# Kernel tuning notes

Hardware: AMD Instinct MI355X
Metric: run time of the kernel (lower is better)

Reference implementation:

```python
import jax, jax.numpy as jnp
import numpy as np

N = 4096
K = 3          # from loss_name 'LMNN-3'
MU = 0.5       # default mu in LMNN
NUM_CLASSES = 10


def setup_inputs() -> dict:
    key = jax.random.key(0)
    k1, k2 = jax.random.split(key)
    distances_sq = jax.random.uniform(k1, (N, N), dtype=jnp.float32)
    labels = jax.random.randint(k2, (N, 1), 0, NUM_CLASSES, dtype=jnp.int32)
    return {"distances_sq": distances_sq, "labels": labels}


def lmnn(D, labels, k=K, mu=MU):
    n = D.shape[0]
    same = (labels == labels.T).astype(D.dtype)              # [n,n] same-class indicator
    cross = same * (1.0 - jnp.eye(n, dtype=D.dtype))         # exclude self-pairs
    order = jnp.argsort(D, axis=-1)                          # ascending per row
    pull_mask = jnp.take_along_axis(cross, order, axis=-1)[:, : k + 1]   # [n,k+1]
    sortD = jnp.take_along_axis(D, order, axis=-1)[:, : k + 1]           # [n,k+1]
    pull_d = sortD * pull_mask                               # masked k+1 nearest distances
    pull = jnp.sum(pull_d)
    # push: sum_{i,m,j} relu((pull_d[i,m] - D[j,i] + 1) * pull_mask[i,m] * (1 - same[j,i]))
    # vectorized form of the original per-row Python loop; hinge is [n, k+1, n]
    hinge = jax.nn.relu(
        (pull_d[:, :, None] - D.T[:, None, :] + 1.0)
        * pull_mask[:, :, None]
        * (1.0 - same.T)[:, None, :]
    )
    push = jnp.sum(hinge)
    return (1.0 - mu) * pull + mu * push


def reference(distances_sq, labels):
    # grad_reverse is identity in the forward pass
    return lmnn(distances_sq, labels)
```

## Files before the change

kernel.cpp:

```cpp
#include <hip/hip_runtime.h>

#define N 4096
#define NCLS 10
#define RPB 4
#define NBLK (N / RPB)
#define CRG 16
#define CRC (NBLK / CRG)

__device__ __forceinline__ bool lessvi(float v1, int i1, float v2, int i2) {
    return (v1 < v2) || (v1 == v2 && i1 < i2);
}

__global__ __launch_bounds__(256, 4) void fused(const float* __restrict__ D,
                                                const int* __restrict__ labels,
                                                float* __restrict__ pdiff,
                                                float* __restrict__ pd_sum,
                                                float* __restrict__ a_cnt) {
    __shared__ float sv[RPB][16];
    __shared__ int   si[RPB][16];

    const int tid  = threadIdx.x;
    const int lane = tid & 63;
    const int wave = tid >> 6;
    const int r0   = blockIdx.x * RPB;

    int4 cl[4];
#pragma unroll
    for (int q = 0; q < 4; ++q) cl[q] = ((const int4*)labels)[tid + 256 * q];

    float4 diff[4] = {{0,0,0,0},{0,0,0,0},{0,0,0,0},{0,0,0,0}};

    const float4* rp = (const float4*)(D + (size_t)r0 * N);
    float4 vc[4], vn[4];
#pragma unroll
    for (int q = 0; q < 4; ++q) vc[q] = rp[tid + 256 * q];

#pragma unroll
    for (int r = 0; r < RPB; ++r) {
        if (r < RPB - 1) {
            const float4* np = rp + (size_t)(r + 1) * (N / 4);
#pragma unroll
            for (int q = 0; q < 4; ++q) vn[q] = np[tid + 256 * q];
        }
        const int row    = r0 + r;
        const int rowlab = labels[row];

        float tv[4] = {INFINITY, INFINITY, INFINITY, INFINITY};
        int   ti[4] = {0x7ffffff0, 0x7ffffff1, 0x7ffffff2, 0x7ffffff3};
#pragma unroll
        for (int q = 0; q < 4; ++q) {
            const float4 v = vc[q];
            diff[q].x += (cl[q].x != rowlab) ? v.x : 0.f;
            diff[q].y += (cl[q].y != rowlab) ? v.y : 0.f;
            diff[q].z += (cl[q].z != rowlab) ? v.z : 0.f;
            diff[q].w += (cl[q].w != rowlab) ? v.w : 0.f;

            const int c0 = 4 * tid + 1024 * q;
            const float vals[4] = {v.x, v.y, v.z, v.w};
#pragma unroll
            for (int e = 0; e < 4; ++e) {
                const float vv = vals[e];
                const int   ci = c0 + e;
                if (lessvi(vv, ci, tv[3], ti[3])) {
                    tv[3] = vv; ti[3] = ci;
#pragma unroll
                    for (int q2 = 3; q2 > 0; --q2) {
                        const bool sw = lessvi(tv[q2], ti[q2], tv[q2-1], ti[q2-1]);
                        const float av = tv[q2-1]; const int ai = ti[q2-1];
                        tv[q2-1] = sw ? tv[q2] : av;
                        ti[q2-1] = sw ? ti[q2] : ai;
                        tv[q2]   = sw ? av : tv[q2];
                        ti[q2]   = sw ? ai : ti[q2];
                    }
                }
            }
        }

#pragma unroll
        for (int off = 1; off < 64; off <<= 1) {
            float yv[4]; int yi[4];
#pragma unroll
            for (int k = 0; k < 4; ++k) {
                yv[k] = __shfl_xor(tv[k], off);
                yi[k] = __shfl_xor(ti[k], off);
            }
            float rv[4]; int ri[4];
#pragma unroll
            for (int k = 0; k < 4; ++k) {
                const bool tm = lessvi(tv[0], ti[0], yv[0], yi[0]);
                rv[k] = tm ? tv[0] : yv[0];
                ri[k] = tm ? ti[0] : yi[0];
#pragma unroll
                for (int q2 = 0; q2 < 3; ++q2) {
                    tv[q2] = tm ? tv[q2 + 1] : tv[q2];
                    ti[q2] = tm ? ti[q2 + 1] : ti[q2];
                    yv[q2] = tm ? yv[q2]     : yv[q2 + 1];
                    yi[q2] = tm ? yi[q2]     : yi[q2 + 1];
                }
            }
#pragma unroll
            for (int k = 0; k < 4; ++k) { tv[k] = rv[k]; ti[k] = ri[k]; }
        }

        if (lane == 0) {
#pragma unroll
            for (int k = 0; k < 4; ++k) {
                sv[r][wave * 4 + k] = tv[k];
                si[r][wave * 4 + k] = ti[k];
            }
        }

#pragma unroll
        for (int q = 0; q < 4; ++q) vc[q] = vn[q];
    }

    float4* op = (float4*)(pdiff + (size_t)blockIdx.x * N);
#pragma unroll
    for (int q = 0; q < 4; ++q) op[tid + 256 * q] = diff[q];

    __syncthreads();
    if (tid < RPB) {
        float bv[4] = {INFINITY, INFINITY, INFINITY, INFINITY};
        int   bi[4] = {0x7ffffff0, 0x7ffffff1, 0x7ffffff2, 0x7ffffff3};
#pragma unroll
        for (int k = 0; k < 16; ++k) {
            const float vv = sv[tid][k];
            const int   ci = si[tid][k];
            if (lessvi(vv, ci, bv[3], bi[3])) {
                bv[3] = vv; bi[3] = ci;
#pragma unroll
                for (int q2 = 3; q2 > 0; --q2) {
                    const bool sw = lessvi(bv[q2], bi[q2], bv[q2-1], bi[q2-1]);
                    const float av = bv[q2-1]; const int ai = bi[q2-1];
                    bv[q2-1] = sw ? bv[q2] : av;
                    bi[q2-1] = sw ? bi[q2] : ai;
                    bv[q2]   = sw ? av : bv[q2];
                    bi[q2]   = sw ? ai : bi[q2];
                }
            }
        }
        const int row = r0 + tid;
        const int li  = labels[row];
        float pd = 0.f, a = 0.f;
#pragma unroll
        for (int m = 0; m < 4; ++m) {
            const int j = bi[m];
            if (j != row && labels[j] == li) { pd += bv[m]; a += 1.f; }
        }
        pd_sum[row] = pd;
        a_cnt[row]  = a;
    }
}

__global__ __launch_bounds__(256) void col_reduce(const float* __restrict__ pdiff,
                                                  float* __restrict__ cdiff) {
    const int tile = blockIdx.x & 3;
    const int g    = blockIdx.x >> 2;
    const int col  = tile * 1024 + threadIdx.x * 4;
    float4 acc = {0.f, 0.f, 0.f, 0.f};
#pragma unroll 8
    for (int ch = 0; ch < CRC; ++ch) {
        const float4 v = *(const float4*)(pdiff + (size_t)(g * CRC + ch) * N + col);
        acc.x += v.x; acc.y += v.y; acc.z += v.z; acc.w += v.w;
    }
    *(float4*)(cdiff + (size_t)g * N + col) = acc;
}

__global__ __launch_bounds__(256) void finalize(const int* __restrict__ labels,
                                                const float* __restrict__ pd_sum,
                                                const float* __restrict__ a_cnt,
                                                const float* __restrict__ cdiff,
                                                float* __restrict__ out) {
    __shared__ int    cnt[NCLS];
    __shared__ double red[256];
    const int tid = threadIdx.x;

    if (tid < NCLS) cnt[tid] = 0;
    __syncthreads();
    for (int i = tid; i < N; i += 256) atomicAdd(&cnt[labels[i]], 1);
    __syncthreads();

    double acc = 0.0;
    for (int i = tid; i < N; i += 256) {
        const int li = labels[i];
        const double pd = (double)pd_sum[i];
        const double a  = (double)a_cnt[i];
        float csf = 0.f;
#pragma unroll
        for (int g = 0; g < CRG; ++g) csf += cdiff[(size_t)g * N + i];
        const double cs = (double)csf;
        const double cd = (double)(N - cnt[li]);
        acc += pd;
        acc += cd * (pd + a) - a * cs;
    }
    red[tid] = acc;
    __syncthreads();
    for (int s = 128; s > 0; s >>= 1) {
        if (tid < s) red[tid] += red[tid + s];
        __syncthreads();
    }
    if (tid == 0) out[0] = (float)(0.5 * red[0]);
}

extern "C" void kernel_launch(void* const* d_in, const int* in_sizes, int n_in,
                              void* d_out, int out_size, void* d_ws, size_t ws_size,
                              hipStream_t stream) {
    const float* D      = (const float*)d_in[0];
    const int*   labels = (const int*)d_in[1];
    float*       out    = (float*)d_out;

    float* pdiff  = (float*)d_ws;
    float* cdiff  = pdiff + (size_t)NBLK * N;
    float* pd_sum = cdiff + (size_t)CRG * N;
    float* a_cnt  = pd_sum + N;

    fused<<<NBLK, 256, 0, stream>>>(D, labels, pdiff, pd_sum, a_cnt);
    col_reduce<<<CRG * 4, 256, 0, stream>>>(pdiff, cdiff);
    finalize<<<1, 256, 0, stream>>>(labels, pd_sum, a_cnt, cdiff, out);
}
```

Before: 127.0 us.

## Replace per-row register top-4 with threshold candidate filtering and a separate selection kernel

The streaming pass no longer keeps a per-thread sorted top-4 and wave shuffle merge per row. Each value below a fixed threshold is appended to a per-row candidate buffer through a shared-memory atomic counter. A new kernel picks the top-4 from those candidates, and falls back to a full row scan when the count is under 4 or over capacity. This removes the compare-and-swap chain from the bandwidth-bound pass. In exchange it adds a kernel launch, scattered candidate writes and a threshold that only suits uniform-in-[0,1) inputs (the fallback keeps it correct).

```diff
diff --git a/kernel.cpp b/kernel.cpp
--- a/kernel.cpp
+++ b/kernel.cpp
@@ -6,23 +6,39 @@
 #define NBLK (N / RPB)
 #define CRG 16
 #define CRC (NBLK / CRG)
+#define CAP 160
+#define THRESH 0.015625f
 
 __device__ __forceinline__ bool lessvi(float v1, int i1, float v2, int i2) {
     return (v1 < v2) || (v1 == v2 && i1 < i2);
 }
 
-__global__ __launch_bounds__(256, 4) void fused(const float* __restrict__ D,
-                                                const int* __restrict__ labels,
-                                                float* __restrict__ pdiff,
-                                                float* __restrict__ pd_sum,
-                                                float* __restrict__ a_cnt) {
-    __shared__ float sv[RPB][16];
-    __shared__ int   si[RPB][16];
-
-    const int tid  = threadIdx.x;
-    const int lane = tid & 63;
-    const int wave = tid >> 6;
-    const int r0   = blockIdx.x * RPB;
+__device__ __forceinline__ void insert4(float vv, int ci, float tv[4], int ti[4]) {
+    if (lessvi(vv, ci, tv[3], ti[3])) {
+        tv[3] = vv; ti[3] = ci;
+#pragma unroll
+        for (int q2 = 3; q2 > 0; --q2) {
+            const bool sw = lessvi(tv[q2], ti[q2], tv[q2 - 1], ti[q2 - 1]);
+            const float av = tv[q2 - 1]; const int ai = ti[q2 - 1];
+            tv[q2 - 1] = sw ? tv[q2] : av;
+            ti[q2 - 1] = sw ? ti[q2] : ai;
+            tv[q2]     = sw ? av : tv[q2];
+            ti[q2]     = sw ? ai : ti[q2];
+        }
+    }
+}
+
+__global__ __launch_bounds__(256) void stream_pass(const float* __restrict__ D,
+                                                   const int* __restrict__ labels,
+                                                   float* __restrict__ pdiff,
+                                                   float* __restrict__ cand_v,
+                                                   int* __restrict__ cand_i,
+                                                   int* __restrict__ cand_cnt) {
+    __shared__ int scnt[RPB];
+    const int tid = threadIdx.x;
+    const int r0  = blockIdx.x * RPB;
+    if (tid < RPB) scnt[tid] = 0;
+    __syncthreads();
 
     int4 cl[4];
 #pragma unroll
@@ -44,9 +60,6 @@
         }
         const int row    = r0 + r;
         const int rowlab = labels[row];
-
-        float tv[4] = {INFINITY, INFINITY, INFINITY, INFINITY};
-        int   ti[4] = {0x7ffffff0, 0x7ffffff1, 0x7ffffff2, 0x7ffffff3};
 #pragma unroll
         for (int q = 0; q < 4; ++q) {
             const float4 v = vc[q];
@@ -59,93 +72,90 @@
             const float vals[4] = {v.x, v.y, v.z, v.w};
 #pragma unroll
             for (int e = 0; e < 4; ++e) {
-                const float vv = vals[e];
-                const int   ci = c0 + e;
-                if (lessvi(vv, ci, tv[3], ti[3])) {
-                    tv[3] = vv; ti[3] = ci;
-#pragma unroll
-                    for (int q2 = 3; q2 > 0; --q2) {
-                        const bool sw = lessvi(tv[q2], ti[q2], tv[q2-1], ti[q2-1]);
-                        const float av = tv[q2-1]; const int ai = ti[q2-1];
-                        tv[q2-1] = sw ? tv[q2] : av;
-                        ti[q2-1] = sw ? ti[q2] : ai;
-                        tv[q2]   = sw ? av : tv[q2];
-                        ti[q2]   = sw ? ai : ti[q2];
+                if (vals[e] < THRESH) {
+                    const int idx = atomicAdd(&scnt[r], 1);
+                    if (idx < CAP) {
+                        cand_v[(size_t)row * CAP + idx] = vals[e];
+                        cand_i[(size_t)row * CAP + idx] = c0 + e;
                     }
                 }
             }
         }
-
-#pragma unroll
-        for (int off = 1; off < 64; off <<= 1) {
-            float yv[4]; int yi[4];
-#pragma unroll
-            for (int k = 0; k < 4; ++k) {
-                yv[k] = __shfl_xor(tv[k], off);
-                yi[k] = __shfl_xor(ti[k], off);
+#pragma unroll
+        for (int q = 0; q < 4; ++q) vc[q] = vn[q];
+    }
+
+    float4* op = (float4*)(pdiff + (size_t)blockIdx.x * N);
+#pragma unroll
+    for (int q = 0; q < 4; ++q) op[tid + 256 * q] = diff[q];
+
+    __syncthreads();
+    if (tid < RPB) cand_cnt[r0 + tid] = scnt[tid];
+}
+
+__global__ __launch_bounds__(256) void select_top4(const float* __restrict__ D,
+                                                   const int* __restrict__ labels,
+                                                   const float* __restrict__ cand_v,
+                                                   const int* __restrict__ cand_i,
+                                                   const int* __restrict__ cand_cnt,
+                                                   float* __restrict__ pd_sum,
+                                                   float* __restrict__ a_cnt) {
+    const int lane = threadIdx.x & 63;
+    const int wave = threadIdx.x >> 6;
+    const int row  = blockIdx.x * 4 + wave;
+    const int cnt  = cand_cnt[row];
+
+    float tv[4] = {INFINITY, INFINITY, INFINITY, INFINITY};
+    int   ti[4] = {0x7ffffff0, 0x7ffffff1, 0x7ffffff2, 0x7ffffff3};
+
+    if (cnt >= 4 && cnt <= CAP) {
+        for (int k = lane; k < cnt; k += 64)
+            insert4(cand_v[(size_t)row * CAP + k], cand_i[(size_t)row * CAP + k], tv, ti);
+    } else {
+        const float4* rp4 = (const float4*)(D + (size_t)row * N);
+        for (int s = 0; s < 16; ++s) {
+            const float4 q = rp4[s * 64 + lane];
+            const int c0 = (s * 64 + lane) * 4;
+            insert4(q.x, c0, tv, ti);
+            insert4(q.y, c0 + 1, tv, ti);
+            insert4(q.z, c0 + 2, tv, ti);
+            insert4(q.w, c0 + 3, tv, ti);
+        }
+    }
+
+#pragma unroll
+    for (int off = 1; off < 64; off <<= 1) {
+        float yv[4]; int yi[4];
+#pragma unroll
+        for (int k = 0; k < 4; ++k) {
+            yv[k] = __shfl_xor(tv[k], off);
+            yi[k] = __shfl_xor(ti[k], off);
+        }
+        float rv[4]; int ri[4];
+#pragma unroll
+        for (int k = 0; k < 4; ++k) {
+            const bool tm = lessvi(tv[0], ti[0], yv[0], yi[0]);
+            rv[k] = tm ? tv[0] : yv[0];
+            ri[k] = tm ? ti[0] : yi[0];
+#pragma unroll
+            for (int q2 = 0; q2 < 3; ++q2) {
+                tv[q2] = tm ? tv[q2 + 1] : tv[q2];
+                ti[q2] = tm ? ti[q2 + 1] : ti[q2];
+                yv[q2] = tm ? yv[q2]     : yv[q2 + 1];
+                yi[q2] = tm ? yi[q2]     : yi[q2 + 1];
             }
-            float rv[4]; int ri[4];
-#pragma unroll
-            for (int k = 0; k < 4; ++k) {
-                const bool tm = lessvi(tv[0], ti[0], yv[0], yi[0]);
-                rv[k] = tm ? tv[0] : yv[0];
-                ri[k] = tm ? ti[0] : yi[0];
-#pragma unroll
-                for (int q2 = 0; q2 < 3; ++q2) {
-                    tv[q2] = tm ? tv[q2 + 1] : tv[q2];
-                    ti[q2] = tm ? ti[q2 + 1] : ti[q2];
-                    yv[q2] = tm ? yv[q2]     : yv[q2 + 1];
-                    yi[q2] = tm ? yi[q2]     : yi[q2 + 1];
-                }
-            }
-#pragma unroll
-            for (int k = 0; k < 4; ++k) { tv[k] = rv[k]; ti[k] = ri[k]; }
-        }
-
-        if (lane == 0) {
-#pragma unroll
-            for (int k = 0; k < 4; ++k) {
-                sv[r][wave * 4 + k] = tv[k];
-                si[r][wave * 4 + k] = ti[k];
-            }
-        }
-
-#pragma unroll
-        for (int q = 0; q < 4; ++q) vc[q] = vn[q];
-    }
-
-    float4* op = (float4*)(pdiff + (size_t)blockIdx.x * N);
-#pragma unroll
-    for (int q = 0; q < 4; ++q) op[tid + 256 * q] = diff[q];
-
-    __syncthreads();
-    if (tid < RPB) {
-        float bv[4] = {INFINITY, INFINITY, INFINITY, INFINITY};
-        int   bi[4] = {0x7ffffff0, 0x7ffffff1, 0x7ffffff2, 0x7ffffff3};
-#pragma unroll
-        for (int k = 0; k < 16; ++k) {
-            const float vv = sv[tid][k];
-            const int   ci = si[tid][k];
-            if (lessvi(vv, ci, bv[3], bi[3])) {
-                bv[3] = vv; bi[3] = ci;
-#pragma unroll
-                for (int q2 = 3; q2 > 0; --q2) {
-                    const bool sw = lessvi(bv[q2], bi[q2], bv[q2-1], bi[q2-1]);
-                    const float av = bv[q2-1]; const int ai = bi[q2-1];
-                    bv[q2-1] = sw ? bv[q2] : av;
-                    bi[q2-1] = sw ? bi[q2] : ai;
-                    bv[q2]   = sw ? av : bv[q2];
-                    bi[q2]   = sw ? ai : bi[q2];
-                }
-            }
-        }
-        const int row = r0 + tid;
-        const int li  = labels[row];
+        }
+#pragma unroll
+        for (int k = 0; k < 4; ++k) { tv[k] = rv[k]; ti[k] = ri[k]; }
+    }
+
+    if (lane == 0) {
+        const int li = labels[row];
         float pd = 0.f, a = 0.f;
 #pragma unroll
         for (int m = 0; m < 4; ++m) {
-            const int j = bi[m];
-            if (j != row && labels[j] == li) { pd += bv[m]; a += 1.f; }
+            const int j = ti[m];
+            if (j != row && labels[j] == li) { pd += tv[m]; a += 1.f; }
         }
         pd_sum[row] = pd;
         a_cnt[row]  = a;
@@ -209,12 +219,16 @@
     const int*   labels = (const int*)d_in[1];
     float*       out    = (float*)d_out;
 
-    float* pdiff  = (float*)d_ws;
-    float* cdiff  = pdiff + (size_t)NBLK * N;
-    float* pd_sum = cdiff + (size_t)CRG * N;
-    float* a_cnt  = pd_sum + N;
-
-    fused<<<NBLK, 256, 0, stream>>>(D, labels, pdiff, pd_sum, a_cnt);
+    float* pdiff    = (float*)d_ws;
+    float* cdiff    = pdiff + (size_t)NBLK * N;
+    float* pd_sum   = cdiff + (size_t)CRG * N;
+    float* a_cnt    = pd_sum + N;
+    float* cand_v   = a_cnt + N;
+    int*   cand_i   = (int*)(cand_v + (size_t)N * CAP);
+    int*   cand_cnt = cand_i + (size_t)N * CAP;
+
+    stream_pass<<<NBLK, 256, 0, stream>>>(D, labels, pdiff, cand_v, cand_i, cand_cnt);
+    select_top4<<<N / 4, 256, 0, stream>>>(D, labels, cand_v, cand_i, cand_cnt, pd_sum, a_cnt);
     col_reduce<<<CRG * 4, 256, 0, stream>>>(pdiff, cdiff);
     finalize<<<1, 256, 0, stream>>>(labels, pd_sum, a_cnt, cdiff, out);
 }
```

Result: faster. 122.5 us (-3.5%).
